# Performance work log

Measured on AMD Instinct MI355X. Metric: run time of the kernel, lower is better.

## Reference

```python
import jax, jax.numpy as jnp
import numpy as np

C = 64
HW = 21 * 21  # 441
NEIGHBOR_K = 3


def setup_inputs() -> dict:
    key = jax.random.key(0)
    k1, k2, k3, k4 = jax.random.split(key, 4)
    B1, B2 = 32, 25
    x1 = jax.random.normal(k1, (B1, C, 21, 21), dtype=jnp.float32)
    x2 = jax.random.normal(k2, (B2, C, 21, 21), dtype=jnp.float32)
    mask1 = jax.random.uniform(k3, (B1, 21, 21), dtype=jnp.float32)
    mask2 = jax.random.uniform(k4, (B2, 21, 21), dtype=jnp.float32)
    return {"x1": x1, "x2": x2, "mask1": mask1, "mask2": mask2}


def reference(x1, x2, mask1, mask2):
    B1 = x1.shape[0]
    B2 = x2.shape[0]
    q = x1.reshape(B1, C, HW)  # (B1, 64, 441) query descriptors
    s = x2.reshape(B2, C, HW)  # (B2, 64, 441) support descriptors
    # per-descriptor L2 norms over channel dim
    qn = jnp.linalg.norm(q, axis=1)  # (B1, 441)
    sn = jnp.linalg.norm(s, axis=1)  # (B2, 441)
    # cosine similarity between every query descriptor and every support descriptor
    inner = jnp.einsum('aci,bcj->abij', q, s)  # (B1, B2, 441, 441)
    sim = inner / (qn[:, None, :, None] * sn[None, :, None, :])
    # mask out invalid spatial positions on both sides
    sim = sim * mask1.reshape(B1, 1, HW, 1) * mask2.reshape(1, B2, 1, HW)
    # top-k nearest support descriptors per query descriptor, sum over all
    topk_vals, _ = jax.lax.top_k(sim, NEIGHBOR_K)  # (B1, B2, 441, k)
    return topk_vals.reshape(B1, B2, -1).sum(axis=2)  # (B1, B2)
```

## Files before the change

### kernel.cpp

```cpp
#include <hip/hip_runtime.h>
#include <math.h>

#define CCH 64
#define HW 441
#define HWP 448
#define NT 28
#define NB2 25
#define PANEL (HWP * CCH)

typedef _Float16 half8 __attribute__((ext_vector_type(8)));
typedef float f32x4 __attribute__((ext_vector_type(4)));

__global__ void normalize_frag_kernel(const float* __restrict__ x1,
                                      const float* __restrict__ m1,
                                      const float* __restrict__ x2,
                                      const float* __restrict__ m2,
                                      _Float16* __restrict__ qh,
                                      _Float16* __restrict__ sh,
                                      int n1rows, int nrows) {
    int idx = blockIdx.x * blockDim.x + threadIdx.x;
    if (idx >= nrows) return;
    const float* x; const float* mk; _Float16* outp; int rb;
    if (idx < n1rows) { x = x1; mk = m1; outp = qh; rb = idx; }
    else             { x = x2; mk = m2; outp = sh; rb = idx - n1rows; }
    int b = rb / HWP, i = rb - b * HWP;
    float vals[CCH];
    if (i < HW) {
        const float* xb = x + (size_t)b * CCH * HW + i;
        float ss = 0.f;
#pragma unroll
        for (int c = 0; c < CCH; ++c) { float v = xb[c * HW]; vals[c] = v; ss += v * v; }
        float scale = mk[b * HW + i] * rsqrtf(ss);
#pragma unroll
        for (int c = 0; c < CCH; ++c) vals[c] *= scale;
    } else {
#pragma unroll
        for (int c = 0; c < CCH; ++c) vals[c] = 0.f;
    }
    _Float16* pb = outp + (size_t)b * PANEL + (i >> 4) * 1024 + (i & 15) * 8;
#pragma unroll
    for (int f = 0; f < 2; ++f) {
#pragma unroll
        for (int qd = 0; qd < 4; ++qd) {
            half8 h;
#pragma unroll
            for (int e = 0; e < 8; ++e) h[e] = (_Float16)vals[f * 32 + qd * 8 + e];
            *(half8*)(pb + f * 512 + qd * 128) = h;
        }
    }
}

__device__ __forceinline__ void top3of4_merge(f32x4 v, float& t0, float& t1, float& t2) {
    float s1 = fmaxf(v[0], v[1]), n1 = fminf(v[0], v[1]);
    float s2 = fmaxf(v[2], v[3]), n2 = fminf(v[2], v[3]);
    float x = fminf(s1, s2), y = fmaxf(n1, n2);
    float b0 = fmaxf(s1, s2);
    float b1 = fmaxf(x, y);
    float b2 = fminf(x, y);
    float m0 = fmaxf(t0, b0), nn0 = fminf(t0, b0);
    float m1 = fmaxf(t1, b1);
    float mt2 = fmaxf(t2, b2);
    t0 = m0;
    t1 = fmaxf(nn0, m1);
    t2 = fmaxf(fminf(nn0, m1), mt2);
}

#define MERGE3(t0, t1, t2, b0, b1, b2)            \
    do {                                          \
        float _m0 = fmaxf(t0, b0);                \
        float _n0 = fminf(t0, b0);                \
        float _m1 = fmaxf(t1, b1);                \
        float _t2 = fmaxf(t2, b2);                \
        t0 = _m0;                                 \
        t1 = fmaxf(_n0, _m1);                     \
        t2 = fmaxf(fminf(_n0, _m1), _t2);         \
    } while (0)

template <int NI>
__device__ __forceinline__ float do_pass(const _Float16* __restrict__ qtiles,
                                         const _Float16* __restrict__ spanel,
                                         int lane, int quad) {
    const float NEG = -1e30f;
    const f32x4 FZ = {0.f, 0.f, 0.f, 0.f};
    half8 bf0[NI], bf1[NI];
#pragma unroll
    for (int t = 0; t < NI; ++t) {
        const _Float16* qp = qtiles + t * 1024 + lane * 8;
        bf0[t] = *(const half8*)qp;
        bf1[t] = *(const half8*)(qp + 512);
    }
    float t0[NI], t1[NI], t2[NI];
#pragma unroll
    for (int t = 0; t < NI; ++t) { t0[t] = NEG; t1[t] = NEG; t2[t] = NEG; }

    for (int jt = 0; jt < NT - 1; ++jt) {
        const _Float16* sp = spanel + jt * 1024 + lane * 8;
        half8 a0 = *(const half8*)sp;
        half8 a1 = *(const half8*)(sp + 512);
#pragma unroll
        for (int t = 0; t < NI; ++t) {
            f32x4 z = __builtin_amdgcn_mfma_f32_16x16x32_f16(a0, bf0[t], FZ, 0, 0, 0);
            z = __builtin_amdgcn_mfma_f32_16x16x32_f16(a1, bf1[t], z, 0, 0, 0);
            top3of4_merge(z, t0[t], t1[t], t2[t]);
        }
    }
    {
        const _Float16* sp = spanel + (NT - 1) * 1024 + lane * 8;
        half8 a0 = *(const half8*)sp;
        half8 a1 = *(const half8*)(sp + 512);
#pragma unroll
        for (int t = 0; t < NI; ++t) {
            f32x4 z = __builtin_amdgcn_mfma_f32_16x16x32_f16(a0, bf0[t], FZ, 0, 0, 0);
            z = __builtin_amdgcn_mfma_f32_16x16x32_f16(a1, bf1[t], z, 0, 0, 0);
#pragma unroll
            for (int r = 0; r < 4; ++r)
                if (quad * 4 + r >= 9) z[r] = NEG;
            top3of4_merge(z, t0[t], t1[t], t2[t]);
        }
    }

    float res = 0.f;
#pragma unroll
    for (int t = 0; t < NI; ++t) {
        float b0 = __shfl_xor(t0[t], 16), b1 = __shfl_xor(t1[t], 16), b2 = __shfl_xor(t2[t], 16);
        MERGE3(t0[t], t1[t], t2[t], b0, b1, b2);
        b0 = __shfl_xor(t0[t], 32); b1 = __shfl_xor(t1[t], 32); b2 = __shfl_xor(t2[t], 32);
        MERGE3(t0[t], t1[t], t2[t], b0, b1, b2);
        res += t0[t] + t1[t] + t2[t];
    }
    return (quad == 0) ? res : 0.f;
}

__global__ __launch_bounds__(128, 6) void sim_topk_mfma(const _Float16* __restrict__ qh,
                                                        const _Float16* __restrict__ sh,
                                                        float* __restrict__ out) {
    __shared__ float s_red[2];
    int blk = blockIdx.x;
    int pair = blk >> 2, g = blk & 3;
    int a = pair / NB2, b = pair - a * NB2;
    int tid = threadIdx.x, wave = tid >> 6, lane = tid & 63, quad = lane >> 4;
    const _Float16* qtiles = qh + (size_t)a * PANEL + (size_t)g * 7 * 1024;
    const _Float16* spanel = sh + (size_t)b * PANEL;

    float wacc = (wave == 0)
                     ? do_pass<4>(qtiles, spanel, lane, quad)
                     : do_pass<3>(qtiles + 4 * 1024, spanel, lane, quad);

#pragma unroll
    for (int off = 32; off > 0; off >>= 1) wacc += __shfl_down(wacc, off);
    if (lane == 0) s_red[wave] = wacc;
    __syncthreads();
    if (tid == 0) atomicAdd(&out[pair], s_red[0] + s_red[1]);
}

extern "C" void kernel_launch(void* const* d_in, const int* in_sizes, int n_in,
                              void* d_out, int out_size, void* d_ws, size_t ws_size,
                              hipStream_t stream) {
    const float* x1 = (const float*)d_in[0];
    const float* x2 = (const float*)d_in[1];
    const float* m1 = (const float*)d_in[2];
    const float* m2 = (const float*)d_in[3];
    float* out = (float*)d_out;

    int B1 = in_sizes[0] / (CCH * HW);
    int B2 = in_sizes[1] / (CCH * HW);

    _Float16* qh = (_Float16*)d_ws;
    _Float16* sh = qh + (size_t)B1 * PANEL;

    hipMemsetAsync(d_out, 0, (size_t)out_size * sizeof(float), stream);

    int n1 = B1 * HWP, ntot = (B1 + B2) * HWP;
    normalize_frag_kernel<<<(ntot + 255) / 256, 256, 0, stream>>>(
        x1, m1, x2, m2, qh, sh, n1, ntot);
    sim_topk_mfma<<<B1 * B2 * 4, 128, 0, stream>>>(qh, sh, out);
}
```

Before: 107.4 us.

## Track top-3 in packed fp16, prefetch support tiles, fold output zeroing into prep

The per-lane top-3 tracking now converts MFMA outputs to packed fp16 pairs and inserts them with packed min/max, which roughly halves the VALU work per tile. The next support tile is also prefetched into registers, and the launch bound occupancy hint drops from 6 to 4. The output memset moves into the normalize kernel, removing one launch, and the LDS reduction with its __syncthreads is replaced by one atomic per wave. Keeping the top-3 in fp16 loses precision in the summed values, which could push results past the tolerance.

```diff
diff --git a/kernel.cpp b/kernel.cpp
--- a/kernel.cpp
+++ b/kernel.cpp
@@ -9,6 +9,7 @@
 #define PANEL (HWP * CCH)
 
 typedef _Float16 half8 __attribute__((ext_vector_type(8)));
+typedef __fp16 h2 __attribute__((ext_vector_type(2)));
 typedef float f32x4 __attribute__((ext_vector_type(4)));
 
 __global__ void normalize_frag_kernel(const float* __restrict__ x1,
@@ -17,8 +18,10 @@
                                       const float* __restrict__ m2,
                                       _Float16* __restrict__ qh,
                                       _Float16* __restrict__ sh,
+                                      float* __restrict__ out, int nout,
                                       int n1rows, int nrows) {
     int idx = blockIdx.x * blockDim.x + threadIdx.x;
+    if (idx < nout) out[idx] = 0.f;
     if (idx >= nrows) return;
     const float* x; const float* mk; _Float16* outp; int rb;
     if (idx < n1rows) { x = x1; mk = m1; outp = qh; rb = idx; }
@@ -50,20 +53,23 @@
     }
 }
 
-__device__ __forceinline__ void top3of4_merge(f32x4 v, float& t0, float& t1, float& t2) {
-    float s1 = fmaxf(v[0], v[1]), n1 = fminf(v[0], v[1]);
-    float s2 = fmaxf(v[2], v[3]), n2 = fminf(v[2], v[3]);
-    float x = fminf(s1, s2), y = fmaxf(n1, n2);
-    float b0 = fmaxf(s1, s2);
-    float b1 = fmaxf(x, y);
-    float b2 = fminf(x, y);
-    float m0 = fmaxf(t0, b0), nn0 = fminf(t0, b0);
-    float m1 = fmaxf(t1, b1);
-    float mt2 = fmaxf(t2, b2);
-    t0 = m0;
-    t1 = fmaxf(nn0, m1);
-    t2 = fmaxf(fminf(nn0, m1), mt2);
+static __device__ __forceinline__ h2 hmax2(h2 a, h2 b) {
+    return __builtin_elementwise_max(a, b);
 }
+static __device__ __forceinline__ h2 hmin2(h2 a, h2 b) {
+    return __builtin_elementwise_min(a, b);
+}
+
+#define PK_INSERT(v, p0, p1, p2)           \
+    do {                                   \
+        h2 _m = hmax2(p0, v);              \
+        h2 _c = hmin2(p0, v);              \
+        p0 = _m;                           \
+        _m = hmax2(p1, _c);                \
+        _c = hmin2(p1, _c);                \
+        p1 = _m;                           \
+        p2 = hmax2(p2, _c);                \
+    } while (0)
 
 #define MERGE3(t0, t1, t2, b0, b1, b2)            \
     do {                                          \
@@ -82,6 +88,7 @@
                                          int lane, int quad) {
     const float NEG = -1e30f;
     const f32x4 FZ = {0.f, 0.f, 0.f, 0.f};
+    const h2 NEGH = {(__fp16)-65504.f, (__fp16)-65504.f};
     half8 bf0[NI], bf1[NI];
 #pragma unroll
     for (int t = 0; t < NI; ++t) {
@@ -89,25 +96,31 @@
         bf0[t] = *(const half8*)qp;
         bf1[t] = *(const half8*)(qp + 512);
     }
-    float t0[NI], t1[NI], t2[NI];
+    h2 p0[NI], p1[NI], p2[NI];
 #pragma unroll
-    for (int t = 0; t < NI; ++t) { t0[t] = NEG; t1[t] = NEG; t2[t] = NEG; }
+    for (int t = 0; t < NI; ++t) { p0[t] = NEGH; p1[t] = NEGH; p2[t] = NEGH; }
+
+    const _Float16* sp = spanel + lane * 8;
+    half8 a0 = *(const half8*)sp;
+    half8 a1 = *(const half8*)(sp + 512);
 
     for (int jt = 0; jt < NT - 1; ++jt) {
-        const _Float16* sp = spanel + jt * 1024 + lane * 8;
-        half8 a0 = *(const half8*)sp;
-        half8 a1 = *(const half8*)(sp + 512);
+        const _Float16* np = sp + (jt + 1) * 1024;
+        half8 na0 = *(const half8*)np;
+        half8 na1 = *(const half8*)(np + 512);
 #pragma unroll
         for (int t = 0; t < NI; ++t) {
             f32x4 z = __builtin_amdgcn_mfma_f32_16x16x32_f16(a0, bf0[t], FZ, 0, 0, 0);
             z = __builtin_amdgcn_mfma_f32_16x16x32_f16(a1, bf1[t], z, 0, 0, 0);
-            top3of4_merge(z, t0[t], t1[t], t2[t]);
+            h2 c02 = __builtin_amdgcn_cvt_pkrtz(z[0], z[2]);
+            h2 c13 = __builtin_amdgcn_cvt_pkrtz(z[1], z[3]);
+            PK_INSERT(c02, p0[t], p1[t], p2[t]);
+            PK_INSERT(c13, p0[t], p1[t], p2[t]);
         }
+        a0 = na0;
+        a1 = na1;
     }
     {
-        const _Float16* sp = spanel + (NT - 1) * 1024 + lane * 8;
-        half8 a0 = *(const half8*)sp;
-        half8 a1 = *(const half8*)(sp + 512);
 #pragma unroll
         for (int t = 0; t < NI; ++t) {
             f32x4 z = __builtin_amdgcn_mfma_f32_16x16x32_f16(a0, bf0[t], FZ, 0, 0, 0);
@@ -115,26 +128,31 @@
 #pragma unroll
             for (int r = 0; r < 4; ++r)
                 if (quad * 4 + r >= 9) z[r] = NEG;
-            top3of4_merge(z, t0[t], t1[t], t2[t]);
+            h2 c02 = __builtin_amdgcn_cvt_pkrtz(z[0], z[2]);
+            h2 c13 = __builtin_amdgcn_cvt_pkrtz(z[1], z[3]);
+            PK_INSERT(c02, p0[t], p1[t], p2[t]);
+            PK_INSERT(c13, p0[t], p1[t], p2[t]);
         }
     }
 
     float res = 0.f;
 #pragma unroll
     for (int t = 0; t < NI; ++t) {
-        float b0 = __shfl_xor(t0[t], 16), b1 = __shfl_xor(t1[t], 16), b2 = __shfl_xor(t2[t], 16);
-        MERGE3(t0[t], t1[t], t2[t], b0, b1, b2);
-        b0 = __shfl_xor(t0[t], 32); b1 = __shfl_xor(t1[t], 32); b2 = __shfl_xor(t2[t], 32);
-        MERGE3(t0[t], t1[t], t2[t], b0, b1, b2);
-        res += t0[t] + t1[t] + t2[t];
+        float t0 = (float)p0[t][0], t1 = (float)p1[t][0], t2 = (float)p2[t][0];
+        float b0 = (float)p0[t][1], b1 = (float)p1[t][1], b2 = (float)p2[t][1];
+        MERGE3(t0, t1, t2, b0, b1, b2);
+        b0 = __shfl_xor(t0, 16); b1 = __shfl_xor(t1, 16); b2 = __shfl_xor(t2, 16);
+        MERGE3(t0, t1, t2, b0, b1, b2);
+        b0 = __shfl_xor(t0, 32); b1 = __shfl_xor(t1, 32); b2 = __shfl_xor(t2, 32);
+        MERGE3(t0, t1, t2, b0, b1, b2);
+        res += t0 + t1 + t2;
     }
     return (quad == 0) ? res : 0.f;
 }
 
-__global__ __launch_bounds__(128, 6) void sim_topk_mfma(const _Float16* __restrict__ qh,
+__global__ __launch_bounds__(128, 4) void sim_topk_mfma(const _Float16* __restrict__ qh,
                                                         const _Float16* __restrict__ sh,
                                                         float* __restrict__ out) {
-    __shared__ float s_red[2];
     int blk = blockIdx.x;
     int pair = blk >> 2, g = blk & 3;
     int a = pair / NB2, b = pair - a * NB2;
@@ -148,9 +166,7 @@
 
 #pragma unroll
     for (int off = 32; off > 0; off >>= 1) wacc += __shfl_down(wacc, off);
-    if (lane == 0) s_red[wave] = wacc;
-    __syncthreads();
-    if (tid == 0) atomicAdd(&out[pair], s_red[0] + s_red[1]);
+    if (lane == 0) atomicAdd(&out[pair], wacc);
 }
 
 extern "C" void kernel_launch(void* const* d_in, const int* in_sizes, int n_in,
@@ -168,10 +184,8 @@
     _Float16* qh = (_Float16*)d_ws;
     _Float16* sh = qh + (size_t)B1 * PANEL;
 
-    hipMemsetAsync(d_out, 0, (size_t)out_size * sizeof(float), stream);
-
     int n1 = B1 * HWP, ntot = (B1 + B2) * HWP;
     normalize_frag_kernel<<<(ntot + 255) / 256, 256, 0, stream>>>(
-        x1, m1, x2, m2, qh, sh, n1, ntot);
+        x1, m1, x2, m2, qh, sh, out, B1 * B2, n1, ntot);
     sim_topk_mfma<<<B1 * B2 * 4, 128, 0, stream>>>(qh, sh, out);
 }
```

Result: faster. 101.5 us (-5.5%).
